# Performance work log

Measured on AMD Instinct MI355X. Metric: run time of the kernel, lower is better.

## Reference

```python
import jax, jax.numpy as jnp
import numpy as np

RC = 5.0          # radial cutoff
NB = 8            # number of Gaussian radial basis functions
NPATH = 11        # graph-conv tensor-product paths (in_way, r_way, n_contract)->out_way
NORM_FACTOR = 10.0


def setup_inputs() -> dict:
    key = jax.random.key(0)
    ks = jax.random.split(key, 24)
    N, E, C = 20000, 200000, 32
    s = 1.0 / np.sqrt(C)
    inp = {
        "rij": jax.random.normal(ks[0], (E, 3), jnp.float32) * 1.5,
        "node_x0": jax.random.normal(ks[1], (N, C), jnp.float32),
        "node_x1": jax.random.normal(ks[2], (N, C, 3), jnp.float32),
        "node_x2": jax.random.normal(ks[3], (N, C, 3, 3), jnp.float32),
        "idx_i": jax.random.randint(ks[4], (E,), 0, N, jnp.int32),
        "idx_j": jax.random.randint(ks[5], (E,), 0, N, jnp.int32),
        # radial filter MLP (rbf -> per-path per-channel filters)
        "W_rbf": jax.random.normal(ks[6], (NB, NPATH * C), jnp.float32) / np.sqrt(NB),
        "b_rbf": jax.random.normal(ks[7], (NPATH * C,), jnp.float32) * 0.1,
        # multi-body self-interaction: channel mixing per way + pair-path couplings
        "Wmix0": jax.random.normal(ks[8], (C, C), jnp.float32) * s,
        "Wmix1": jax.random.normal(ks[9], (C, C), jnp.float32) * s,
        "Wmix2": jax.random.normal(ks[10], (C, C), jnp.float32) * s,
        "coupling": jax.random.normal(ks[11], (8, C), jnp.float32) * 0.1,
        # gated nonlinearity params (gates computed from way-0 features)
        "Wg0": jax.random.normal(ks[12], (C, C), jnp.float32) * s,
        "Wg1": jax.random.normal(ks[13], (C, C), jnp.float32) * s,
        "Wg2": jax.random.normal(ks[14], (C, C), jnp.float32) * s,
        "bg0": jnp.zeros((C,), jnp.float32),
        "bg1": jnp.zeros((C,), jnp.float32),
        "bg2": jnp.zeros((C,), jnp.float32),
    }
    return inp


def _forward(rij, node_x0, node_x1, node_x2, idx_i, idx_j,
             W_rbf, b_rbf, Wmix0, Wmix1, Wmix2, coupling,
             Wg0, Wg1, Wg2, bg0, bg1, bg2):
    N, C = node_x0.shape
    # --- radial filters ---
    d = jnp.maximum(jnp.linalg.norm(rij, axis=-1), 1e-6)            # [E]
    rhat = rij / d[:, None]                                         # [E,3]
    centers = jnp.linspace(0.0, RC, NB)
    rbf = jnp.exp(-((d[:, None] - centers) ** 2) / 0.25)            # [E,NB]
    fc = 0.5 * (jnp.cos(jnp.pi * jnp.minimum(d, RC) / RC) + 1.0)    # cosine cutoff
    filt = ((rbf @ W_rbf + b_rbf) * fc[:, None]).reshape(-1, NPATH, C)  # [E,P,C]

    # --- graph conv (conv_mode='node_j'): gather neighbor tensors, tensor-product with rhat ---
    xj0 = node_x0[idx_j]                                            # [E,C]
    xj1 = node_x1[idx_j]                                            # [E,C,3]
    xj2 = node_x2[idx_j]                                            # [E,C,3,3]
    x1r = jnp.einsum('eca,ea->ec', xj1, rhat)                       # v.rhat

    m0 = filt[:, 0] * xj0
    m0 += filt[:, 5] * x1r
    m0 += filt[:, 10] * jnp.einsum('ecab,ea,eb->ec', xj2, rhat, rhat)

    m1 = jnp.einsum('ec,ea->eca', filt[:, 1] * xj0, rhat)
    m1 += filt[:, 3][:, :, None] * xj1
    m1 += jnp.einsum('ec,ea->eca', filt[:, 6] * x1r, rhat)
    m1 += filt[:, 8][:, :, None] * jnp.einsum('ecab,eb->eca', xj2, rhat)

    m2 = jnp.einsum('ec,ea,eb->ecab', filt[:, 2] * xj0, rhat, rhat)
    m2 += jnp.einsum('eca,eb->ecab', filt[:, 4][:, :, None] * xj1, rhat)
    m2 += filt[:, 7][:, :, None, None] * xj2
    m2 += filt[:, 9][:, :, None, None] * jnp.einsum('ecab,eb,ed->ecad', xj2, rhat, rhat)

    # --- scatter-add aggregation per way + normalization ---
    a0 = jax.ops.segment_sum(m0, idx_i, num_segments=N) / NORM_FACTOR
    a1 = jax.ops.segment_sum(m1, idx_i, num_segments=N) / NORM_FACTOR
    a2 = jax.ops.segment_sum(m2, idx_i, num_segments=N) / NORM_FACTOR

    # --- multi-body self-interaction (channel mix + pairwise tensor contractions) ---
    cp = coupling
    y0 = a0 @ Wmix0 \
        + cp[0] * (a0 * a0) \
        + cp[3] * jnp.einsum('nca,nca->nc', a1, a1) \
        + cp[6] * jnp.einsum('ncab,ncab->nc', a2, a2)
    y1 = jnp.einsum('nca,cd->nda', a1, Wmix1) \
        + cp[1][None, :, None] * a0[:, :, None] * a1 \
        + cp[5][None, :, None] * jnp.einsum('ncab,ncb->nca', a2, a1)
    y2 = jnp.einsum('ncab,cd->ndab', a2, Wmix2) \
        + cp[2][None, :, None, None] * a0[:, :, None, None] * a2 \
        + cp[4][None, :, None, None] * jnp.einsum('nca,ncb->ncab', a1, a1) \
        + cp[7][None, :, None, None] * jnp.einsum('ncab,ncbd->ncad', a2, a2)

    # --- gated nonlinearity (scalar channel drives gates for higher ways) ---
    z0 = jax.nn.silu(y0 @ Wg0 + bg0)
    z1 = y1 * jax.nn.silu(y0 @ Wg1 + bg1)[:, :, None]
    z2 = y2 * jax.nn.silu(y0 @ Wg2 + bg2)[:, :, None, None]

    # --- residual add (res_add) ---
    o0 = node_x0 + z0
    o1 = node_x1 + z1
    o2 = node_x2 + z2
    # pack dict {0,1,2} outputs into one array [N,C,1+3+9]
    return jnp.concatenate([o0[:, :, None], o1, o2.reshape(N, C, 9)], axis=-1)


def reference(rij, node_x0, node_x1, node_x2, idx_i, idx_j,
              W_rbf, b_rbf, Wmix0, Wmix1, Wmix2, coupling,
              Wg0, Wg1, Wg2, bg0, bg1, bg2):
    return _forward(rij, node_x0, node_x1, node_x2, idx_i, idx_j,
                    W_rbf, b_rbf, Wmix0, Wmix1, Wmix2, coupling,
                    Wg0, Wg1, Wg2, bg0, bg1, bg2)
```

## Files before the change

### kernel.cpp

```cpp
#include <hip/hip_runtime.h>
#include <cmath>

#define CH 32
#define NBASIS 8
#define NPATH 11
#define NF 13
#define NPF (NF * CH)
#define MAXDEG 40
#define NW 4

typedef unsigned int u32;
typedef __fp16 half2_t __attribute__((ext_vector_type(2)));

__device__ __forceinline__ float silu_f(float x) {
    return x / (1.0f + __expf(-x));
}

__device__ __forceinline__ u32 bf16r(float x) {
    return (__float_as_uint(x) + 0x8000u) >> 16;
}
__device__ __forceinline__ float bf16lo(u32 w) {
    return __uint_as_float(w << 16);
}
__device__ __forceinline__ float bf16hi(u32 w) {
    return __uint_as_float(w & 0xffff0000u);
}

__device__ __forceinline__ u32 f16pk(float a, float b) {
    union { half2_t h; u32 u; } cv;
    cv.h = __builtin_amdgcn_cvt_pkrtz(a, b);
    return cv.u;
}
__device__ __forceinline__ half2_t ash2(u32 w) {
    union { u32 u; half2_t h; } cv; cv.u = w; return cv.h;
}

#if __has_builtin(__builtin_amdgcn_fdot2)
__device__ __forceinline__ float dot2f(u32 a, u32 b, float c) {
    return __builtin_amdgcn_fdot2(ash2(a), ash2(b), c, false);
}
#else
__device__ __forceinline__ float dot2f(u32 a, u32 b, float c) {
    half2_t ha = ash2(a), hb = ash2(b);
    c = fmaf((float)ha.x, (float)hb.x, c);
    c = fmaf((float)ha.y, (float)hb.y, c);
    return c;
}
#endif

__device__ __forceinline__ void gload_lds16(const void* g, void* l) {
    __builtin_amdgcn_global_load_lds(
        (const __attribute__((address_space(1))) void*)g,
        (__attribute__((address_space(3))) void*)l, 16, 0, 0);
}

__global__ __launch_bounds__(256) void repack_kernel(
    const float* __restrict__ x0,
    const float* __restrict__ x1,
    const float* __restrict__ x2,
    uint4* __restrict__ xph4,
    int*   __restrict__ cnt,
    int N)
{
    int t = blockIdx.x * 256 + threadIdx.x;
    if (t < N) cnt[t] = 0;
    if (t >= N * CH) return;

    float f[13];
    f[0] = x0[t];
    const float* p1 = x1 + (size_t)t * 3;
#pragma unroll
    for (int a = 0; a < 3; a++) f[1 + a] = p1[a];
    const float* p2 = x2 + (size_t)t * 9;
#pragma unroll
    for (int q = 0; q < 9; q++) f[4 + q] = p2[q];

    u32 d[8];
#pragma unroll
    for (int qp = 0; qp < 6; qp++)
        d[qp] = bf16r(f[2 * qp]) | (bf16r(f[2 * qp + 1]) << 16);
    d[6] = bf16r(f[12]);
    d[7] = 0u;
    uint4* xo = xph4 + (size_t)t * 2;
    xo[0] = make_uint4(d[0], d[1], d[2], d[3]);
    xo[1] = make_uint4(d[4], d[5], d[6], d[7]);
}

__global__ __launch_bounds__(256) void fill_slots(
    const float* __restrict__ rij,
    const int*   __restrict__ idx_i,
    const int*   __restrict__ idx_j,
    int*    __restrict__ cnt,
    float4* __restrict__ recs,
    int E)
{
    int e = blockIdx.x * 256 + threadIdx.x;
    if (e >= E) return;

    float rx = rij[e * 3 + 0], ry = rij[e * 3 + 1], rz = rij[e * 3 + 2];
    float dn = sqrtf(rx * rx + ry * ry + rz * rz);
    float d = fmaxf(dn, 1e-6f);
    float inv = 1.0f / d;

    float rbf[NBASIS];
#pragma unroll
    for (int k = 0; k < NBASIS; k++) {
        float ck = 5.0f * (float)k / (float)(NBASIS - 1);
        float del = d - ck;
        rbf[k] = __expf(-4.0f * del * del);
    }
    float dc = fminf(d, 5.0f);
    float fc = 0.5f * (__cosf((float)M_PI * dc * 0.2f) + 1.0f);
    float scale = fc * 0.1f;

    int i = idx_i[e];
    int pos = atomicAdd(&cnt[i], 1);
    if (pos >= MAXDEG) return;

    u32 w3  = ((u32)idx_j[e] << 16) | bf16r(scale);
    u32 p01 = f16pk(rbf[0] * scale, rbf[1] * scale);
    u32 p23 = f16pk(rbf[2] * scale, rbf[3] * scale);
    u32 p45 = f16pk(rbf[4] * scale, rbf[5] * scale);
    u32 p67 = f16pk(rbf[6] * scale, rbf[7] * scale);

    float4* r = recs + 2 * (size_t)(i * MAXDEG + pos);
    r[0] = make_float4(rx * inv, ry * inv, rz * inv, __uint_as_float(w3));
    r[1] = make_float4(__uint_as_float(p01), __uint_as_float(p23),
                       __uint_as_float(p45), __uint_as_float(p67));
}

__global__ __launch_bounds__(256, 1) void edge_kernel(
    const float4*   __restrict__ recs,
    const uint4*    __restrict__ xph4,
    const int*      __restrict__ cnt,
    const float*    __restrict__ W_rbf,
    const float*    __restrict__ b_rbf,
    float* __restrict__ anode,
    int N)
{
    __shared__ uint4  sW4[NPATH * CH];
    __shared__ float4 srec[NW][MAXDEG * 2];

    int tid  = threadIdx.x;
    int wid  = tid >> 6;
    int lane = tid & 63;
    int half = lane >> 5;
    int c    = lane & 31;
    int n    = blockIdx.x * NW + wid;
    bool valid = (n < N);
    int nn = valid ? n : (N - 1);

    const char* gbase = (const char*)(recs + 2 * (size_t)nn * MAXDEG);
    {
        char* lbase = (char*)&srec[wid][0];
        gload_lds16(gbase + lane * 16, lbase);
        if (lane < 16)
            gload_lds16(gbase + 1024 + lane * 16, lbase + 1024);
    }

    const u32* recw = (const u32*)gbase;
    u32 w30 = recw[half * 8 + 3];
    u32 w31 = recw[(half + 2) * 8 + 3];
    u32 w32 = recw[(half + 4) * 8 + 3];
    int deg_g = cnt[nn];

#pragma unroll
    for (int i = 0; i < 2; i++) {
        int idx = tid + i * 256;
        if (idx < NPATH * CH) {
            int cc = idx & 31, p = idx >> 5;
            const float* w = W_rbf + p * CH + cc;
            uint4 v;
            v.x = f16pk(w[0 * NPATH * CH], w[1 * NPATH * CH]);
            v.y = f16pk(w[2 * NPATH * CH], w[3 * NPATH * CH]);
            v.z = f16pk(w[4 * NPATH * CH], w[5 * NPATH * CH]);
            v.w = f16pk(w[6 * NPATH * CH], w[7 * NPATH * CH]);
            sW4[idx] = v;
        }
    }

    float breg[NPATH];
#pragma unroll
    for (int p = 0; p < NPATH; p++) breg[p] = b_rbf[p * CH + c];

    auto gath = [&](uint4& ga, uint4& gb, u32 w3) {
        int j = (int)(w3 >> 16);
        j = j < N ? j : N - 1;
        const uint4* g = xph4 + (((size_t)j * CH + c) << 1);
        ga = g[0];
        gb = g[1];
    };

    uint4 G0a, G0b, G1a, G1b, G2a, G2b;
    gath(G0a, G0b, w30);
    gath(G1a, G1b, w31);
    gath(G2a, G2b, w32);

    __syncthreads();
    if (!valid) return;

    int deg = deg_g < MAXDEG ? deg_g : MAXDEG;

    int s0 = half, s1 = half + 2, s2 = half + 4;
    bool v0 = s0 < deg, v1 = s1 < deg, v2 = s2 < deg;

    float A0 = 0.0f, A1[3] = {0, 0, 0}, A2[9] = {0, 0, 0, 0, 0, 0, 0, 0, 0};

    const uint4* sW4c = sW4 + c;

    auto compute = [&](float4 ra, float4 rb4, uint4 ga, uint4 gb) {
        float G[13];
        G[0]  = bf16lo(ga.x); G[1]  = bf16hi(ga.x);
        G[2]  = bf16lo(ga.y); G[3]  = bf16hi(ga.y);
        G[4]  = bf16lo(ga.z); G[5]  = bf16hi(ga.z);
        G[6]  = bf16lo(ga.w); G[7]  = bf16hi(ga.w);
        G[8]  = bf16lo(gb.x); G[9]  = bf16hi(gb.x);
        G[10] = bf16lo(gb.y); G[11] = bf16hi(gb.y);
        G[12] = bf16lo(gb.z);

        float scale = bf16lo(__float_as_uint(ra.w));
        u32 pb0 = __float_as_uint(rb4.x), pb1 = __float_as_uint(rb4.y),
            pb2 = __float_as_uint(rb4.z), pb3 = __float_as_uint(rb4.w);

        float fv[NPATH];
#pragma unroll
        for (int p = 0; p < NPATH; p++) {
            uint4 wp = sW4c[p * CH];
            float acc = scale * breg[p];
            acc = dot2f(pb0, wp.x, acc);
            acc = dot2f(pb1, wp.y, acc);
            acc = dot2f(pb2, wp.z, acc);
            acc = dot2f(pb3, wp.w, acc);
            fv[p] = acc;
        }

        float hv[3] = {ra.x, ra.y, ra.z};
        float xj0 = G[0];
        float xv[3] = {G[1], G[2], G[3]};
        float x1r = xv[0] * hv[0] + xv[1] * hv[1] + xv[2] * hv[2];
        float x2r[3];
#pragma unroll
        for (int a = 0; a < 3; a++)
            x2r[a] = G[4 + a * 3 + 0] * hv[0] + G[4 + a * 3 + 1] * hv[1]
                   + G[4 + a * 3 + 2] * hv[2];
        float x2rr = x2r[0] * hv[0] + x2r[1] * hv[1] + x2r[2] * hv[2];

        A0 += fv[0] * xj0 + fv[5] * x1r + fv[10] * x2rr;

        float s01 = fv[1] * xj0 + fv[6] * x1r;
#pragma unroll
        for (int a = 0; a < 3; a++)
            A1[a] += s01 * hv[a] + fv[3] * xv[a] + fv[8] * x2r[a];

        float f2x = fv[2] * xj0;
#pragma unroll
        for (int a = 0; a < 3; a++) {
            float w = f2x * hv[a] + fv[4] * xv[a] + fv[9] * x2r[a];
#pragma unroll
            for (int b = 0; b < 3; b++)
                A2[a * 3 + b] += w * hv[b] + fv[7] * G[4 + a * 3 + b];
        }
    };

    const float4* sr = srec[wid];

    while (v0) {
        bool n0 = (s0 + 6 < deg);
        bool n1 = v1 && (s1 + 6 < deg);
        bool n2 = v2 && (s2 + 6 < deg);

        float4 ra0 = sr[2 * s0], rb0 = sr[2 * s0 + 1];
        int t0 = s0 + 6 < MAXDEG ? s0 + 6 : MAXDEG - 1;
        u32 w0n = __float_as_uint(sr[2 * t0].w);
        float4 ra1, rb1, ra2, rb2;
        u32 w1n = 0, w2n = 0;
        if (v1) {
            ra1 = sr[2 * s1]; rb1 = sr[2 * s1 + 1];
            int t1 = s1 + 6 < MAXDEG ? s1 + 6 : MAXDEG - 1;
            w1n = __float_as_uint(sr[2 * t1].w);
        }
        if (v2) {
            ra2 = sr[2 * s2]; rb2 = sr[2 * s2 + 1];
            int t2 = s2 + 6 < MAXDEG ? s2 + 6 : MAXDEG - 1;
            w2n = __float_as_uint(sr[2 * t2].w);
        }

        compute(ra0, rb0, G0a, G0b);
        if (n0) gath(G0a, G0b, w0n);
        s0 += 6; v0 = n0;

        if (v1) {
            compute(ra1, rb1, G1a, G1b);
            if (n1) gath(G1a, G1b, w1n);
            s1 += 6; v1 = n1;
        }
        if (v2) {
            compute(ra2, rb2, G2a, G2b);
            if (n2) gath(G2a, G2b, w2n);
            s2 += 6; v2 = n2;
        }
    }

    A0 += __shfl_xor(A0, 32);
#pragma unroll
    for (int a = 0; a < 3; a++) A1[a] += __shfl_xor(A1[a], 32);
#pragma unroll
    for (int q = 0; q < 9; q++) A2[q] += __shfl_xor(A2[q], 32);

    float* an = anode + (size_t)n * NPF;
    if (half == 0) {
        an[c] = A0;
#pragma unroll
        for (int a = 0; a < 3; a++) an[(1 + a) * CH + c] = A1[a];
    } else {
#pragma unroll
        for (int q = 0; q < 9; q++) an[(4 + q) * CH + c] = A2[q];
    }
}

__global__ __launch_bounds__(256) void node_update(
    const float* __restrict__ anode,
    const float* __restrict__ x0,
    const float* __restrict__ x1,
    const float* __restrict__ x2,
    const float* __restrict__ Wmix0, const float* __restrict__ Wmix1, const float* __restrict__ Wmix2,
    const float* __restrict__ coupling,
    const float* __restrict__ Wg0, const float* __restrict__ Wg1, const float* __restrict__ Wg2,
    const float* __restrict__ bg0, const float* __restrict__ bg1, const float* __restrict__ bg2,
    float* __restrict__ out, int N)
{
    __shared__ float sW[6][CH * CH];
    __shared__ float sA[8 * NPF];
    __shared__ float sy0[8][CH];
    __shared__ float ob[8 * NPF];

    int tid  = threadIdx.x;
    int nl   = tid >> 5;
    int d    = tid & 31;
    int nbase = blockIdx.x * 8;
    int n    = nbase + nl;
    int nsafe = n < N ? n : N - 1;

#pragma unroll
    for (int r = 0; r < 4; r++) {
        int idx = r * 256 + tid;
        sW[0][idx] = Wmix0[idx];
        sW[1][idx] = Wmix1[idx];
        sW[2][idx] = Wmix2[idx];
        sW[3][idx] = Wg0[idx];
        sW[4][idx] = Wg1[idx];
        sW[5][idx] = Wg2[idx];
    }
    int limit = (N - nbase) * NPF;
    if (limit > 8 * NPF) limit = 8 * NPF;
    {
        const float* ab = anode + (size_t)nbase * NPF;
#pragma unroll
        for (int r = 0; r < 13; r++) {
            int idx = r * 256 + tid;
            sA[idx] = (idx < limit) ? ab[idx] : 0.0f;
        }
    }
    __syncthreads();

    const float* An = sA + nl * NPF;

    float a0d = An[0 * CH + d];
    float a1d[3], a2d[9];
#pragma unroll
    for (int a = 0; a < 3; a++) a1d[a] = An[(1 + a) * CH + d];
#pragma unroll
    for (int q = 0; q < 9; q++) a2d[q] = An[(4 + q) * CH + d];

    float y0 = 0.0f;
#pragma unroll 8
    for (int cc = 0; cc < CH; cc++)
        y0 = fmaf(An[cc], sW[0][cc * CH + d], y0);
    {
        float cp0 = coupling[0 * CH + d], cp3 = coupling[3 * CH + d], cp6 = coupling[6 * CH + d];
        float n1v = a1d[0] * a1d[0] + a1d[1] * a1d[1] + a1d[2] * a1d[2];
        float n2v = 0.0f;
#pragma unroll
        for (int q = 0; q < 9; q++) n2v = fmaf(a2d[q], a2d[q], n2v);
        y0 += cp0 * a0d * a0d + cp3 * n1v + cp6 * n2v;
    }
    sy0[nl][d] = y0;
    __syncthreads();

    float y1[3] = {0, 0, 0};
    float y2[9] = {0, 0, 0, 0, 0, 0, 0, 0, 0};
    float g0 = bg0[d], g1 = bg1[d], g2 = bg2[d];
#pragma unroll 4
    for (int cc = 0; cc < CH; cc++) {
        float w1 = sW[1][cc * CH + d];
        float w2 = sW[2][cc * CH + d];
#pragma unroll
        for (int a = 0; a < 3; a++) y1[a] = fmaf(An[(1 + a) * CH + cc], w1, y1[a]);
#pragma unroll
        for (int q = 0; q < 9; q++) y2[q] = fmaf(An[(4 + q) * CH + cc], w2, y2[q]);
        float yv = sy0[nl][cc];
        g0 = fmaf(yv, sW[3][cc * CH + d], g0);
        g1 = fmaf(yv, sW[4][cc * CH + d], g1);
        g2 = fmaf(yv, sW[5][cc * CH + d], g2);
    }

    {
        float cp1 = coupling[1 * CH + d], cp5 = coupling[5 * CH + d];
#pragma unroll
        for (int a = 0; a < 3; a++) {
            float a2a1 = a2d[a * 3 + 0] * a1d[0] + a2d[a * 3 + 1] * a1d[1] + a2d[a * 3 + 2] * a1d[2];
            y1[a] += cp1 * a0d * a1d[a] + cp5 * a2a1;
        }
        float cp2 = coupling[2 * CH + d], cp4 = coupling[4 * CH + d], cp7 = coupling[7 * CH + d];
#pragma unroll
        for (int a = 0; a < 3; a++) {
#pragma unroll
            for (int b = 0; b < 3; b++) {
                float a2a2 = a2d[a * 3 + 0] * a2d[0 * 3 + b] + a2d[a * 3 + 1] * a2d[1 * 3 + b]
                           + a2d[a * 3 + 2] * a2d[2 * 3 + b];
                y2[a * 3 + b] += cp2 * a0d * a2d[a * 3 + b] + cp4 * a1d[a] * a1d[b] + cp7 * a2a2;
            }
        }
    }

    g0 = silu_f(g0);
    g1 = silu_f(g1);
    g2 = silu_f(g2);

    {
        const float* xs0 = x0 + (size_t)nsafe * CH;
        const float* xs1 = x1 + ((size_t)nsafe * CH + d) * 3;
        const float* xs2 = x2 + ((size_t)nsafe * CH + d) * 9;
        float* o = ob + nl * NPF + d * NF;
        o[0] = xs0[d] + g0;
#pragma unroll
        for (int a = 0; a < 3; a++)
            o[1 + a] = xs1[a] + y1[a] * g1;
#pragma unroll
        for (int q = 0; q < 9; q++)
            o[4 + q] = xs2[q] + y2[q] * g2;
    }
    __syncthreads();

    float* op = out + (size_t)nbase * NPF;
#pragma unroll
    for (int r = 0; r < 13; r++) {
        int idx = r * 256 + tid;
        if (idx < limit) op[idx] = ob[idx];
    }
}

extern "C" void kernel_launch(void* const* d_in, const int* in_sizes, int n_in,
                              void* d_out, int out_size, void* d_ws, size_t ws_size,
                              hipStream_t stream) {
    const float* rij      = (const float*)d_in[0];
    const float* x0       = (const float*)d_in[1];
    const float* x1       = (const float*)d_in[2];
    const float* x2       = (const float*)d_in[3];
    const int*   idx_i    = (const int*)d_in[4];
    const int*   idx_j    = (const int*)d_in[5];
    const float* W_rbf    = (const float*)d_in[6];
    const float* b_rbf    = (const float*)d_in[7];
    const float* Wmix0    = (const float*)d_in[8];
    const float* Wmix1    = (const float*)d_in[9];
    const float* Wmix2    = (const float*)d_in[10];
    const float* coupling = (const float*)d_in[11];
    const float* Wg0      = (const float*)d_in[12];
    const float* Wg1      = (const float*)d_in[13];
    const float* Wg2      = (const float*)d_in[14];
    const float* bg0      = (const float*)d_in[15];
    const float* bg1      = (const float*)d_in[16];
    const float* bg2      = (const float*)d_in[17];

    int E = in_sizes[4];
    int N = in_sizes[1] / CH;

    float4* recs  = (float4*)d_ws;
    uint4*  xph4  = (uint4*)(recs + 2 * (size_t)N * MAXDEG);
    int*    cnt   = (int*)(xph4 + (size_t)N * CH * 2);
    float*  anode = (float*)d_out;

    int ablocks = (N * CH + 255) / 256;
    repack_kernel<<<ablocks, 256, 0, stream>>>(x0, x1, x2, xph4, cnt, N);

    int eblocks = (E + 255) / 256;
    fill_slots<<<eblocks, 256, 0, stream>>>(rij, idx_i, idx_j, cnt, recs, E);

    edge_kernel<<<(N + NW - 1) / NW, 256, 0, stream>>>(recs, xph4, cnt,
                                                       W_rbf, b_rbf, anode, N);

    node_update<<<(N + 7) / 8, 256, 0, stream>>>(anode, x0, x1, x2,
                                                 Wmix0, Wmix1, Wmix2, coupling,
                                                 Wg0, Wg1, Wg2, bg0, bg1, bg2,
                                                 (float*)d_out, N);
}
```

Before: 223.7 us.

## Fuse all four stages into one persistent cooperative kernel with grid syncs

Replaces the repack, slot-fill, edge and node-update kernels with a single cooperative persistent kernel. Grid-wide syncs separate the phases, and a shared-memory buffer is reused across them. The aim is to remove launch overhead and inter-kernel gaps. In exchange it takes on grid-sync costs and limits occupancy to one block per CU, with launch_bounds(256,1) and large shared memory, for every phase. The node-update phase must now also run safely in place on the output buffer across persistent loops.

```diff
diff --git a/kernel.cpp b/kernel.cpp
--- a/kernel.cpp
+++ b/kernel.cpp
@@ -1,5 +1,8 @@
 #include <hip/hip_runtime.h>
+#include <hip/hip_cooperative_groups.h>
 #include <cmath>
+
+namespace cg = cooperative_groups;
 
 #define CH 32
 #define NBASIS 8
@@ -12,6 +15,16 @@
 typedef unsigned int u32;
 typedef __fp16 half2_t __attribute__((ext_vector_type(2)));
 
+#define SM_W4_BYTES   (NPATH * CH * 16)
+#define SM_SREC_OFF   SM_W4_BYTES
+#define SM_SREC_BYTES (NW * MAXDEG * 2 * 16)
+#define SM_W6_BYTES   (6 * CH * CH * 4)
+#define SM_SA_OFF     SM_W6_BYTES
+#define SM_SA_BYTES   (8 * NPF * 4)
+#define SM_SY0_OFF    (SM_SA_OFF + SM_SA_BYTES)
+#define SM_SY0_BYTES  (8 * CH * 4)
+#define SMEM_TOTAL    (SM_SY0_OFF + SM_SY0_BYTES)
+
 __device__ __forceinline__ float silu_f(float x) {
     return x / (1.0f + __expf(-x));
 }
@@ -54,399 +67,407 @@
         (__attribute__((address_space(3))) void*)l, 16, 0, 0);
 }
 
-__global__ __launch_bounds__(256) void repack_kernel(
+__global__ __launch_bounds__(256, 1) void mega_kernel(
+    const float* __restrict__ rij,
     const float* __restrict__ x0,
     const float* __restrict__ x1,
     const float* __restrict__ x2,
-    uint4* __restrict__ xph4,
-    int*   __restrict__ cnt,
-    int N)
-{
-    int t = blockIdx.x * 256 + threadIdx.x;
-    if (t < N) cnt[t] = 0;
-    if (t >= N * CH) return;
-
-    float f[13];
-    f[0] = x0[t];
-    const float* p1 = x1 + (size_t)t * 3;
-#pragma unroll
-    for (int a = 0; a < 3; a++) f[1 + a] = p1[a];
-    const float* p2 = x2 + (size_t)t * 9;
-#pragma unroll
-    for (int q = 0; q < 9; q++) f[4 + q] = p2[q];
-
-    u32 d[8];
-#pragma unroll
-    for (int qp = 0; qp < 6; qp++)
-        d[qp] = bf16r(f[2 * qp]) | (bf16r(f[2 * qp + 1]) << 16);
-    d[6] = bf16r(f[12]);
-    d[7] = 0u;
-    uint4* xo = xph4 + (size_t)t * 2;
-    xo[0] = make_uint4(d[0], d[1], d[2], d[3]);
-    xo[1] = make_uint4(d[4], d[5], d[6], d[7]);
-}
-
-__global__ __launch_bounds__(256) void fill_slots(
-    const float* __restrict__ rij,
     const int*   __restrict__ idx_i,
     const int*   __restrict__ idx_j,
+    const float* __restrict__ W_rbf,
+    const float* __restrict__ b_rbf,
+    const float* __restrict__ Wmix0, const float* __restrict__ Wmix1,
+    const float* __restrict__ Wmix2,
+    const float* __restrict__ coupling,
+    const float* __restrict__ Wg0, const float* __restrict__ Wg1,
+    const float* __restrict__ Wg2,
+    const float* __restrict__ bg0, const float* __restrict__ bg1,
+    const float* __restrict__ bg2,
+    float4* __restrict__ recs,
+    uint4*  __restrict__ xph4,
     int*    __restrict__ cnt,
-    float4* __restrict__ recs,
-    int E)
+    float*  __restrict__ out,
+    int N, int E)
 {
-    int e = blockIdx.x * 256 + threadIdx.x;
-    if (e >= E) return;
-
-    float rx = rij[e * 3 + 0], ry = rij[e * 3 + 1], rz = rij[e * 3 + 2];
-    float dn = sqrtf(rx * rx + ry * ry + rz * rz);
-    float d = fmaxf(dn, 1e-6f);
-    float inv = 1.0f / d;
-
-    float rbf[NBASIS];
-#pragma unroll
-    for (int k = 0; k < NBASIS; k++) {
-        float ck = 5.0f * (float)k / (float)(NBASIS - 1);
-        float del = d - ck;
-        rbf[k] = __expf(-4.0f * del * del);
+    cg::grid_group gg = cg::this_grid();
+    __shared__ __align__(16) char smem[SMEM_TOTAL];
+
+    int tid  = threadIdx.x;
+    int bid  = blockIdx.x;
+    int nblk = gridDim.x;
+    int gstride = nblk * 256;
+    int gt = bid * 256 + tid;
+
+    for (int i = gt; i < N; i += gstride) cnt[i] = 0;
+    gg.sync();
+
+    for (int t = gt; t < N * CH; t += gstride) {
+        float f[13];
+        f[0] = x0[t];
+        const float* p1 = x1 + (size_t)t * 3;
+#pragma unroll
+        for (int a = 0; a < 3; a++) f[1 + a] = p1[a];
+        const float* p2 = x2 + (size_t)t * 9;
+#pragma unroll
+        for (int q = 0; q < 9; q++) f[4 + q] = p2[q];
+
+        u32 d[8];
+#pragma unroll
+        for (int qp = 0; qp < 6; qp++)
+            d[qp] = bf16r(f[2 * qp]) | (bf16r(f[2 * qp + 1]) << 16);
+        d[6] = bf16r(f[12]);
+        d[7] = 0u;
+        uint4* xo = xph4 + (size_t)t * 2;
+        xo[0] = make_uint4(d[0], d[1], d[2], d[3]);
+        xo[1] = make_uint4(d[4], d[5], d[6], d[7]);
     }
-    float dc = fminf(d, 5.0f);
-    float fc = 0.5f * (__cosf((float)M_PI * dc * 0.2f) + 1.0f);
-    float scale = fc * 0.1f;
-
-    int i = idx_i[e];
-    int pos = atomicAdd(&cnt[i], 1);
-    if (pos >= MAXDEG) return;
-
-    u32 w3  = ((u32)idx_j[e] << 16) | bf16r(scale);
-    u32 p01 = f16pk(rbf[0] * scale, rbf[1] * scale);
-    u32 p23 = f16pk(rbf[2] * scale, rbf[3] * scale);
-    u32 p45 = f16pk(rbf[4] * scale, rbf[5] * scale);
-    u32 p67 = f16pk(rbf[6] * scale, rbf[7] * scale);
-
-    float4* r = recs + 2 * (size_t)(i * MAXDEG + pos);
-    r[0] = make_float4(rx * inv, ry * inv, rz * inv, __uint_as_float(w3));
-    r[1] = make_float4(__uint_as_float(p01), __uint_as_float(p23),
-                       __uint_as_float(p45), __uint_as_float(p67));
-}
-
-__global__ __launch_bounds__(256, 1) void edge_kernel(
-    const float4*   __restrict__ recs,
-    const uint4*    __restrict__ xph4,
-    const int*      __restrict__ cnt,
-    const float*    __restrict__ W_rbf,
-    const float*    __restrict__ b_rbf,
-    float* __restrict__ anode,
-    int N)
-{
-    __shared__ uint4  sW4[NPATH * CH];
-    __shared__ float4 srec[NW][MAXDEG * 2];
-
-    int tid  = threadIdx.x;
-    int wid  = tid >> 6;
-    int lane = tid & 63;
-    int half = lane >> 5;
-    int c    = lane & 31;
-    int n    = blockIdx.x * NW + wid;
-    bool valid = (n < N);
-    int nn = valid ? n : (N - 1);
-
-    const char* gbase = (const char*)(recs + 2 * (size_t)nn * MAXDEG);
+
+    for (int e = gt; e < E; e += gstride) {
+        float rx = rij[e * 3 + 0], ry = rij[e * 3 + 1], rz = rij[e * 3 + 2];
+        float dn = sqrtf(rx * rx + ry * ry + rz * rz);
+        float d = fmaxf(dn, 1e-6f);
+        float inv = 1.0f / d;
+
+        float rbf[NBASIS];
+#pragma unroll
+        for (int k = 0; k < NBASIS; k++) {
+            float ck = 5.0f * (float)k / (float)(NBASIS - 1);
+            float del = d - ck;
+            rbf[k] = __expf(-4.0f * del * del);
+        }
+        float dc = fminf(d, 5.0f);
+        float fc = 0.5f * (__cosf((float)M_PI * dc * 0.2f) + 1.0f);
+        float scale = fc * 0.1f;
+
+        int i = idx_i[e];
+        int pos = atomicAdd(&cnt[i], 1);
+        if (pos >= MAXDEG) continue;
+
+        u32 w3  = ((u32)idx_j[e] << 16) | bf16r(scale);
+        u32 p01 = f16pk(rbf[0] * scale, rbf[1] * scale);
+        u32 p23 = f16pk(rbf[2] * scale, rbf[3] * scale);
+        u32 p45 = f16pk(rbf[4] * scale, rbf[5] * scale);
+        u32 p67 = f16pk(rbf[6] * scale, rbf[7] * scale);
+
+        float4* r = recs + 2 * (size_t)(i * MAXDEG + pos);
+        r[0] = make_float4(rx * inv, ry * inv, rz * inv, __uint_as_float(w3));
+        r[1] = make_float4(__uint_as_float(p01), __uint_as_float(p23),
+                           __uint_as_float(p45), __uint_as_float(p67));
+    }
+    gg.sync();
+
     {
-        char* lbase = (char*)&srec[wid][0];
-        gload_lds16(gbase + lane * 16, lbase);
-        if (lane < 16)
-            gload_lds16(gbase + 1024 + lane * 16, lbase + 1024);
-    }
-
-    const u32* recw = (const u32*)gbase;
-    u32 w30 = recw[half * 8 + 3];
-    u32 w31 = recw[(half + 2) * 8 + 3];
-    u32 w32 = recw[(half + 4) * 8 + 3];
-    int deg_g = cnt[nn];
-
-#pragma unroll
-    for (int i = 0; i < 2; i++) {
-        int idx = tid + i * 256;
-        if (idx < NPATH * CH) {
-            int cc = idx & 31, p = idx >> 5;
+        uint4*  sW4  = (uint4*)smem;
+        float4* srec = (float4*)(smem + SM_SREC_OFF);
+
+        for (int i = tid; i < NPATH * CH; i += 256) {
+            int cc = i & 31, p = i >> 5;
             const float* w = W_rbf + p * CH + cc;
             uint4 v;
             v.x = f16pk(w[0 * NPATH * CH], w[1 * NPATH * CH]);
             v.y = f16pk(w[2 * NPATH * CH], w[3 * NPATH * CH]);
             v.z = f16pk(w[4 * NPATH * CH], w[5 * NPATH * CH]);
             v.w = f16pk(w[6 * NPATH * CH], w[7 * NPATH * CH]);
-            sW4[idx] = v;
+            sW4[i] = v;
+        }
+
+        int wid  = tid >> 6;
+        int lane = tid & 63;
+        int half = lane >> 5;
+        int c    = lane & 31;
+
+        float breg[NPATH];
+#pragma unroll
+        for (int p = 0; p < NPATH; p++) breg[p] = b_rbf[p * CH + c];
+
+        const uint4* sW4c = sW4 + c;
+        float4* srw = srec + (size_t)wid * (MAXDEG * 2);
+
+        auto gath = [&](uint4& ga, uint4& gb, u32 w3) {
+            int j = (int)(w3 >> 16);
+            j = j < N ? j : N - 1;
+            const uint4* g = xph4 + (((size_t)j * CH + c) << 1);
+            ga = g[0];
+            gb = g[1];
+        };
+
+        int ngroups = (N + NW - 1) / NW;
+        for (int g = bid; g < ngroups; g += nblk) {
+            __syncthreads();
+
+            int n = g * NW + wid;
+            bool valid = (n < N);
+            int nn = valid ? n : (N - 1);
+
+            const char* gbase = (const char*)(recs + 2 * (size_t)nn * MAXDEG);
+            {
+                char* lbase = (char*)srw;
+                gload_lds16(gbase + lane * 16, lbase);
+                if (lane < 16)
+                    gload_lds16(gbase + 1024 + lane * 16, lbase + 1024);
+            }
+
+            const u32* recw = (const u32*)gbase;
+            u32 w30 = recw[half * 8 + 3];
+            u32 w31 = recw[(half + 2) * 8 + 3];
+            u32 w32 = recw[(half + 4) * 8 + 3];
+            int deg_g = cnt[nn];
+
+            uint4 G0a, G0b, G1a, G1b, G2a, G2b;
+            gath(G0a, G0b, w30);
+            gath(G1a, G1b, w31);
+            gath(G2a, G2b, w32);
+
+            __syncthreads();
+
+            int deg = valid ? (deg_g < MAXDEG ? deg_g : MAXDEG) : 0;
+
+            int s0 = half, s1 = half + 2, s2 = half + 4;
+            bool v0 = s0 < deg, v1 = s1 < deg, v2 = s2 < deg;
+
+            float A0 = 0.0f, A1[3] = {0, 0, 0};
+            float A2[9] = {0, 0, 0, 0, 0, 0, 0, 0, 0};
+
+            auto compute = [&](float4 ra, float4 rb4, uint4 ga, uint4 gb) {
+                float G[13];
+                G[0]  = bf16lo(ga.x); G[1]  = bf16hi(ga.x);
+                G[2]  = bf16lo(ga.y); G[3]  = bf16hi(ga.y);
+                G[4]  = bf16lo(ga.z); G[5]  = bf16hi(ga.z);
+                G[6]  = bf16lo(ga.w); G[7]  = bf16hi(ga.w);
+                G[8]  = bf16lo(gb.x); G[9]  = bf16hi(gb.x);
+                G[10] = bf16lo(gb.y); G[11] = bf16hi(gb.y);
+                G[12] = bf16lo(gb.z);
+
+                float scale = bf16lo(__float_as_uint(ra.w));
+                u32 pb0 = __float_as_uint(rb4.x), pb1 = __float_as_uint(rb4.y),
+                    pb2 = __float_as_uint(rb4.z), pb3 = __float_as_uint(rb4.w);
+
+                float fv[NPATH];
+#pragma unroll
+                for (int p = 0; p < NPATH; p++) {
+                    uint4 wp = sW4c[p * CH];
+                    float acc = scale * breg[p];
+                    acc = dot2f(pb0, wp.x, acc);
+                    acc = dot2f(pb1, wp.y, acc);
+                    acc = dot2f(pb2, wp.z, acc);
+                    acc = dot2f(pb3, wp.w, acc);
+                    fv[p] = acc;
+                }
+
+                float hv[3] = {ra.x, ra.y, ra.z};
+                float xj0 = G[0];
+                float xv[3] = {G[1], G[2], G[3]};
+                float x1r = xv[0] * hv[0] + xv[1] * hv[1] + xv[2] * hv[2];
+                float x2r[3];
+#pragma unroll
+                for (int a = 0; a < 3; a++)
+                    x2r[a] = G[4 + a * 3 + 0] * hv[0] + G[4 + a * 3 + 1] * hv[1]
+                           + G[4 + a * 3 + 2] * hv[2];
+                float x2rr = x2r[0] * hv[0] + x2r[1] * hv[1] + x2r[2] * hv[2];
+
+                A0 += fv[0] * xj0 + fv[5] * x1r + fv[10] * x2rr;
+
+                float s01 = fv[1] * xj0 + fv[6] * x1r;
+#pragma unroll
+                for (int a = 0; a < 3; a++)
+                    A1[a] += s01 * hv[a] + fv[3] * xv[a] + fv[8] * x2r[a];
+
+                float f2x = fv[2] * xj0;
+#pragma unroll
+                for (int a = 0; a < 3; a++) {
+                    float w = f2x * hv[a] + fv[4] * xv[a] + fv[9] * x2r[a];
+#pragma unroll
+                    for (int b = 0; b < 3; b++)
+                        A2[a * 3 + b] += w * hv[b] + fv[7] * G[4 + a * 3 + b];
+                }
+            };
+
+            const float4* sr = srw;
+
+            while (v0) {
+                bool n0 = (s0 + 6 < deg);
+                bool n1 = v1 && (s1 + 6 < deg);
+                bool n2 = v2 && (s2 + 6 < deg);
+
+                float4 ra0 = sr[2 * s0], rb0 = sr[2 * s0 + 1];
+                int t0 = s0 + 6 < MAXDEG ? s0 + 6 : MAXDEG - 1;
+                u32 w0n = __float_as_uint(sr[2 * t0].w);
+                float4 ra1, rb1, ra2, rb2;
+                u32 w1n = 0, w2n = 0;
+                if (v1) {
+                    ra1 = sr[2 * s1]; rb1 = sr[2 * s1 + 1];
+                    int t1 = s1 + 6 < MAXDEG ? s1 + 6 : MAXDEG - 1;
+                    w1n = __float_as_uint(sr[2 * t1].w);
+                }
+                if (v2) {
+                    ra2 = sr[2 * s2]; rb2 = sr[2 * s2 + 1];
+                    int t2 = s2 + 6 < MAXDEG ? s2 + 6 : MAXDEG - 1;
+                    w2n = __float_as_uint(sr[2 * t2].w);
+                }
+
+                compute(ra0, rb0, G0a, G0b);
+                if (n0) gath(G0a, G0b, w0n);
+                s0 += 6; v0 = n0;
+
+                if (v1) {
+                    compute(ra1, rb1, G1a, G1b);
+                    if (n1) gath(G1a, G1b, w1n);
+                    s1 += 6; v1 = n1;
+                }
+                if (v2) {
+                    compute(ra2, rb2, G2a, G2b);
+                    if (n2) gath(G2a, G2b, w2n);
+                    s2 += 6; v2 = n2;
+                }
+            }
+
+            if (valid) {
+                A0 += __shfl_xor(A0, 32);
+#pragma unroll
+                for (int a = 0; a < 3; a++) A1[a] += __shfl_xor(A1[a], 32);
+#pragma unroll
+                for (int q = 0; q < 9; q++) A2[q] += __shfl_xor(A2[q], 32);
+
+                float* an = out + (size_t)n * NPF;
+                if (half == 0) {
+                    an[c] = A0;
+#pragma unroll
+                    for (int a = 0; a < 3; a++) an[(1 + a) * CH + c] = A1[a];
+                } else {
+#pragma unroll
+                    for (int q = 0; q < 9; q++) an[(4 + q) * CH + c] = A2[q];
+                }
+            }
         }
     }
-
-    float breg[NPATH];
-#pragma unroll
-    for (int p = 0; p < NPATH; p++) breg[p] = b_rbf[p * CH + c];
-
-    auto gath = [&](uint4& ga, uint4& gb, u32 w3) {
-        int j = (int)(w3 >> 16);
-        j = j < N ? j : N - 1;
-        const uint4* g = xph4 + (((size_t)j * CH + c) << 1);
-        ga = g[0];
-        gb = g[1];
-    };
-
-    uint4 G0a, G0b, G1a, G1b, G2a, G2b;
-    gath(G0a, G0b, w30);
-    gath(G1a, G1b, w31);
-    gath(G2a, G2b, w32);
-
-    __syncthreads();
-    if (!valid) return;
-
-    int deg = deg_g < MAXDEG ? deg_g : MAXDEG;
-
-    int s0 = half, s1 = half + 2, s2 = half + 4;
-    bool v0 = s0 < deg, v1 = s1 < deg, v2 = s2 < deg;
-
-    float A0 = 0.0f, A1[3] = {0, 0, 0}, A2[9] = {0, 0, 0, 0, 0, 0, 0, 0, 0};
-
-    const uint4* sW4c = sW4 + c;
-
-    auto compute = [&](float4 ra, float4 rb4, uint4 ga, uint4 gb) {
-        float G[13];
-        G[0]  = bf16lo(ga.x); G[1]  = bf16hi(ga.x);
-        G[2]  = bf16lo(ga.y); G[3]  = bf16hi(ga.y);
-        G[4]  = bf16lo(ga.z); G[5]  = bf16hi(ga.z);
-        G[6]  = bf16lo(ga.w); G[7]  = bf16hi(ga.w);
-        G[8]  = bf16lo(gb.x); G[9]  = bf16hi(gb.x);
-        G[10] = bf16lo(gb.y); G[11] = bf16hi(gb.y);
-        G[12] = bf16lo(gb.z);
-
-        float scale = bf16lo(__float_as_uint(ra.w));
-        u32 pb0 = __float_as_uint(rb4.x), pb1 = __float_as_uint(rb4.y),
-            pb2 = __float_as_uint(rb4.z), pb3 = __float_as_uint(rb4.w);
-
-        float fv[NPATH];
-#pragma unroll
-        for (int p = 0; p < NPATH; p++) {
-            uint4 wp = sW4c[p * CH];
-            float acc = scale * breg[p];
-            acc = dot2f(pb0, wp.x, acc);
-            acc = dot2f(pb1, wp.y, acc);
-            acc = dot2f(pb2, wp.z, acc);
-            acc = dot2f(pb3, wp.w, acc);
-            fv[p] = acc;
+    gg.sync();
+
+    {
+        float* sW6  = (float*)smem;
+        float* sA   = (float*)(smem + SM_SA_OFF);
+        float* sy0v = (float*)(smem + SM_SY0_OFF);
+
+#pragma unroll
+        for (int r = 0; r < 4; r++) {
+            int idx = r * 256 + tid;
+            sW6[0 * 1024 + idx] = Wmix0[idx];
+            sW6[1 * 1024 + idx] = Wmix1[idx];
+            sW6[2 * 1024 + idx] = Wmix2[idx];
+            sW6[3 * 1024 + idx] = Wg0[idx];
+            sW6[4 * 1024 + idx] = Wg1[idx];
+            sW6[5 * 1024 + idx] = Wg2[idx];
         }
 
-        float hv[3] = {ra.x, ra.y, ra.z};
-        float xj0 = G[0];
-        float xv[3] = {G[1], G[2], G[3]};
-        float x1r = xv[0] * hv[0] + xv[1] * hv[1] + xv[2] * hv[2];
-        float x2r[3];
-#pragma unroll
-        for (int a = 0; a < 3; a++)
-            x2r[a] = G[4 + a * 3 + 0] * hv[0] + G[4 + a * 3 + 1] * hv[1]
-                   + G[4 + a * 3 + 2] * hv[2];
-        float x2rr = x2r[0] * hv[0] + x2r[1] * hv[1] + x2r[2] * hv[2];
-
-        A0 += fv[0] * xj0 + fv[5] * x1r + fv[10] * x2rr;
-
-        float s01 = fv[1] * xj0 + fv[6] * x1r;
-#pragma unroll
-        for (int a = 0; a < 3; a++)
-            A1[a] += s01 * hv[a] + fv[3] * xv[a] + fv[8] * x2r[a];
-
-        float f2x = fv[2] * xj0;
-#pragma unroll
-        for (int a = 0; a < 3; a++) {
-            float w = f2x * hv[a] + fv[4] * xv[a] + fv[9] * x2r[a];
-#pragma unroll
-            for (int b = 0; b < 3; b++)
-                A2[a * 3 + b] += w * hv[b] + fv[7] * G[4 + a * 3 + b];
+        int nl = tid >> 5;
+        int d  = tid & 31;
+
+        int noct = (N + 7) / 8;
+        for (int g = bid; g < noct; g += nblk) {
+            __syncthreads();
+
+            int nbase = g * 8;
+            int n     = nbase + nl;
+            int nsafe = n < N ? n : N - 1;
+            int limit = (N - nbase) * NPF;
+            if (limit > 8 * NPF) limit = 8 * NPF;
+
+            const float* ab = out + (size_t)nbase * NPF;
+#pragma unroll
+            for (int r = 0; r < 13; r++) {
+                int idx = r * 256 + tid;
+                sA[idx] = (idx < limit) ? ab[idx] : 0.0f;
+            }
+            __syncthreads();
+
+            const float* An = sA + nl * NPF;
+
+            float a0d = An[0 * CH + d];
+            float a1d[3], a2d[9];
+#pragma unroll
+            for (int a = 0; a < 3; a++) a1d[a] = An[(1 + a) * CH + d];
+#pragma unroll
+            for (int q = 0; q < 9; q++) a2d[q] = An[(4 + q) * CH + d];
+
+            float y0 = 0.0f;
+#pragma unroll 8
+            for (int cc = 0; cc < CH; cc++)
+                y0 = fmaf(An[cc], sW6[0 * 1024 + cc * CH + d], y0);
+            {
+                float cp0 = coupling[0 * CH + d], cp3 = coupling[3 * CH + d],
+                      cp6 = coupling[6 * CH + d];
+                float n1v = a1d[0] * a1d[0] + a1d[1] * a1d[1] + a1d[2] * a1d[2];
+                float n2v = 0.0f;
+#pragma unroll
+                for (int q = 0; q < 9; q++) n2v = fmaf(a2d[q], a2d[q], n2v);
+                y0 += cp0 * a0d * a0d + cp3 * n1v + cp6 * n2v;
+            }
+            sy0v[nl * CH + d] = y0;
+            __syncthreads();
+
+            float y1[3] = {0, 0, 0};
+            float y2[9] = {0, 0, 0, 0, 0, 0, 0, 0, 0};
+            float g0 = bg0[d], g1 = bg1[d], g2 = bg2[d];
+#pragma unroll 4
+            for (int cc = 0; cc < CH; cc++) {
+                float w1 = sW6[1 * 1024 + cc * CH + d];
+                float w2 = sW6[2 * 1024 + cc * CH + d];
+#pragma unroll
+                for (int a = 0; a < 3; a++)
+                    y1[a] = fmaf(An[(1 + a) * CH + cc], w1, y1[a]);
+#pragma unroll
+                for (int q = 0; q < 9; q++)
+                    y2[q] = fmaf(An[(4 + q) * CH + cc], w2, y2[q]);
+                float yv = sy0v[nl * CH + cc];
+                g0 = fmaf(yv, sW6[3 * 1024 + cc * CH + d], g0);
+                g1 = fmaf(yv, sW6[4 * 1024 + cc * CH + d], g1);
+                g2 = fmaf(yv, sW6[5 * 1024 + cc * CH + d], g2);
+            }
+
+            {
+                float cp1 = coupling[1 * CH + d], cp5 = coupling[5 * CH + d];
+#pragma unroll
+                for (int a = 0; a < 3; a++) {
+                    float a2a1 = a2d[a * 3 + 0] * a1d[0] + a2d[a * 3 + 1] * a1d[1]
+                               + a2d[a * 3 + 2] * a1d[2];
+                    y1[a] += cp1 * a0d * a1d[a] + cp5 * a2a1;
+                }
+                float cp2 = coupling[2 * CH + d], cp4 = coupling[4 * CH + d],
+                      cp7 = coupling[7 * CH + d];
+#pragma unroll
+                for (int a = 0; a < 3; a++) {
+#pragma unroll
+                    for (int b = 0; b < 3; b++) {
+                        float a2a2 = a2d[a * 3 + 0] * a2d[0 * 3 + b]
+                                   + a2d[a * 3 + 1] * a2d[1 * 3 + b]
+                                   + a2d[a * 3 + 2] * a2d[2 * 3 + b];
+                        y2[a * 3 + b] += cp2 * a0d * a2d[a * 3 + b]
+                                       + cp4 * a1d[a] * a1d[b] + cp7 * a2a2;
+                    }
+                }
+            }
+
+            g0 = silu_f(g0);
+            g1 = silu_f(g1);
+            g2 = silu_f(g2);
+
+            if (n < N) {
+                const float* xs0 = x0 + (size_t)nsafe * CH;
+                const float* xs1 = x1 + ((size_t)nsafe * CH + d) * 3;
+                const float* xs2 = x2 + ((size_t)nsafe * CH + d) * 9;
+                float* o = out + (size_t)n * NPF + d * NF;
+                float r0 = xs0[d] + g0;
+                float r1[3], r2[9];
+#pragma unroll
+                for (int a = 0; a < 3; a++) r1[a] = xs1[a] + y1[a] * g1;
+#pragma unroll
+                for (int q = 0; q < 9; q++) r2[q] = xs2[q] + y2[q] * g2;
+                o[0] = r0;
+#pragma unroll
+                for (int a = 0; a < 3; a++) o[1 + a] = r1[a];
+#pragma unroll
+                for (int q = 0; q < 9; q++) o[4 + q] = r2[q];
+            }
         }
-    };
-
-    const float4* sr = srec[wid];
-
-    while (v0) {
-        bool n0 = (s0 + 6 < deg);
-        bool n1 = v1 && (s1 + 6 < deg);
-        bool n2 = v2 && (s2 + 6 < deg);
-
-        float4 ra0 = sr[2 * s0], rb0 = sr[2 * s0 + 1];
-        int t0 = s0 + 6 < MAXDEG ? s0 + 6 : MAXDEG - 1;
-        u32 w0n = __float_as_uint(sr[2 * t0].w);
-        float4 ra1, rb1, ra2, rb2;
-        u32 w1n = 0, w2n = 0;
-        if (v1) {
-            ra1 = sr[2 * s1]; rb1 = sr[2 * s1 + 1];
-            int t1 = s1 + 6 < MAXDEG ? s1 + 6 : MAXDEG - 1;
-            w1n = __float_as_uint(sr[2 * t1].w);
-        }
-        if (v2) {
-            ra2 = sr[2 * s2]; rb2 = sr[2 * s2 + 1];
-            int t2 = s2 + 6 < MAXDEG ? s2 + 6 : MAXDEG - 1;
-            w2n = __float_as_uint(sr[2 * t2].w);
-        }
-
-        compute(ra0, rb0, G0a, G0b);
-        if (n0) gath(G0a, G0b, w0n);
-        s0 += 6; v0 = n0;
-
-        if (v1) {
-            compute(ra1, rb1, G1a, G1b);
-            if (n1) gath(G1a, G1b, w1n);
-            s1 += 6; v1 = n1;
-        }
-        if (v2) {
-            compute(ra2, rb2, G2a, G2b);
-            if (n2) gath(G2a, G2b, w2n);
-            s2 += 6; v2 = n2;
-        }
-    }
-
-    A0 += __shfl_xor(A0, 32);
-#pragma unroll
-    for (int a = 0; a < 3; a++) A1[a] += __shfl_xor(A1[a], 32);
-#pragma unroll
-    for (int q = 0; q < 9; q++) A2[q] += __shfl_xor(A2[q], 32);
-
-    float* an = anode + (size_t)n * NPF;
-    if (half == 0) {
-        an[c] = A0;
-#pragma unroll
-        for (int a = 0; a < 3; a++) an[(1 + a) * CH + c] = A1[a];
-    } else {
-#pragma unroll
-        for (int q = 0; q < 9; q++) an[(4 + q) * CH + c] = A2[q];
-    }
-}
-
-__global__ __launch_bounds__(256) void node_update(
-    const float* __restrict__ anode,
-    const float* __restrict__ x0,
-    const float* __restrict__ x1,
-    const float* __restrict__ x2,
-    const float* __restrict__ Wmix0, const float* __restrict__ Wmix1, const float* __restrict__ Wmix2,
-    const float* __restrict__ coupling,
-    const float* __restrict__ Wg0, const float* __restrict__ Wg1, const float* __restrict__ Wg2,
-    const float* __restrict__ bg0, const float* __restrict__ bg1, const float* __restrict__ bg2,
-    float* __restrict__ out, int N)
-{
-    __shared__ float sW[6][CH * CH];
-    __shared__ float sA[8 * NPF];
-    __shared__ float sy0[8][CH];
-    __shared__ float ob[8 * NPF];
-
-    int tid  = threadIdx.x;
-    int nl   = tid >> 5;
-    int d    = tid & 31;
-    int nbase = blockIdx.x * 8;
-    int n    = nbase + nl;
-    int nsafe = n < N ? n : N - 1;
-
-#pragma unroll
-    for (int r = 0; r < 4; r++) {
-        int idx = r * 256 + tid;
-        sW[0][idx] = Wmix0[idx];
-        sW[1][idx] = Wmix1[idx];
-        sW[2][idx] = Wmix2[idx];
-        sW[3][idx] = Wg0[idx];
-        sW[4][idx] = Wg1[idx];
-        sW[5][idx] = Wg2[idx];
-    }
-    int limit = (N - nbase) * NPF;
-    if (limit > 8 * NPF) limit = 8 * NPF;
-    {
-        const float* ab = anode + (size_t)nbase * NPF;
-#pragma unroll
-        for (int r = 0; r < 13; r++) {
-            int idx = r * 256 + tid;
-            sA[idx] = (idx < limit) ? ab[idx] : 0.0f;
-        }
-    }
-    __syncthreads();
-
-    const float* An = sA + nl * NPF;
-
-    float a0d = An[0 * CH + d];
-    float a1d[3], a2d[9];
-#pragma unroll
-    for (int a = 0; a < 3; a++) a1d[a] = An[(1 + a) * CH + d];
-#pragma unroll
-    for (int q = 0; q < 9; q++) a2d[q] = An[(4 + q) * CH + d];
-
-    float y0 = 0.0f;
-#pragma unroll 8
-    for (int cc = 0; cc < CH; cc++)
-        y0 = fmaf(An[cc], sW[0][cc * CH + d], y0);
-    {
-        float cp0 = coupling[0 * CH + d], cp3 = coupling[3 * CH + d], cp6 = coupling[6 * CH + d];
-        float n1v = a1d[0] * a1d[0] + a1d[1] * a1d[1] + a1d[2] * a1d[2];
-        float n2v = 0.0f;
-#pragma unroll
-        for (int q = 0; q < 9; q++) n2v = fmaf(a2d[q], a2d[q], n2v);
-        y0 += cp0 * a0d * a0d + cp3 * n1v + cp6 * n2v;
-    }
-    sy0[nl][d] = y0;
-    __syncthreads();
-
-    float y1[3] = {0, 0, 0};
-    float y2[9] = {0, 0, 0, 0, 0, 0, 0, 0, 0};
-    float g0 = bg0[d], g1 = bg1[d], g2 = bg2[d];
-#pragma unroll 4
-    for (int cc = 0; cc < CH; cc++) {
-        float w1 = sW[1][cc * CH + d];
-        float w2 = sW[2][cc * CH + d];
-#pragma unroll
-        for (int a = 0; a < 3; a++) y1[a] = fmaf(An[(1 + a) * CH + cc], w1, y1[a]);
-#pragma unroll
-        for (int q = 0; q < 9; q++) y2[q] = fmaf(An[(4 + q) * CH + cc], w2, y2[q]);
-        float yv = sy0[nl][cc];
-        g0 = fmaf(yv, sW[3][cc * CH + d], g0);
-        g1 = fmaf(yv, sW[4][cc * CH + d], g1);
-        g2 = fmaf(yv, sW[5][cc * CH + d], g2);
-    }
-
-    {
-        float cp1 = coupling[1 * CH + d], cp5 = coupling[5 * CH + d];
-#pragma unroll
-        for (int a = 0; a < 3; a++) {
-            float a2a1 = a2d[a * 3 + 0] * a1d[0] + a2d[a * 3 + 1] * a1d[1] + a2d[a * 3 + 2] * a1d[2];
-            y1[a] += cp1 * a0d * a1d[a] + cp5 * a2a1;
-        }
-        float cp2 = coupling[2 * CH + d], cp4 = coupling[4 * CH + d], cp7 = coupling[7 * CH + d];
-#pragma unroll
-        for (int a = 0; a < 3; a++) {
-#pragma unroll
-            for (int b = 0; b < 3; b++) {
-                float a2a2 = a2d[a * 3 + 0] * a2d[0 * 3 + b] + a2d[a * 3 + 1] * a2d[1 * 3 + b]
-                           + a2d[a * 3 + 2] * a2d[2 * 3 + b];
-                y2[a * 3 + b] += cp2 * a0d * a2d[a * 3 + b] + cp4 * a1d[a] * a1d[b] + cp7 * a2a2;
-            }
-        }
-    }
-
-    g0 = silu_f(g0);
-    g1 = silu_f(g1);
-    g2 = silu_f(g2);
-
-    {
-        const float* xs0 = x0 + (size_t)nsafe * CH;
-        const float* xs1 = x1 + ((size_t)nsafe * CH + d) * 3;
-        const float* xs2 = x2 + ((size_t)nsafe * CH + d) * 9;
-        float* o = ob + nl * NPF + d * NF;
-        o[0] = xs0[d] + g0;
-#pragma unroll
-        for (int a = 0; a < 3; a++)
-            o[1 + a] = xs1[a] + y1[a] * g1;
-#pragma unroll
-        for (int q = 0; q < 9; q++)
-            o[4 + q] = xs2[q] + y2[q] * g2;
-    }
-    __syncthreads();
-
-    float* op = out + (size_t)nbase * NPF;
-#pragma unroll
-    for (int r = 0; r < 13; r++) {
-        int idx = r * 256 + tid;
-        if (idx < limit) op[idx] = ob[idx];
     }
 }
 
@@ -475,22 +496,38 @@
     int E = in_sizes[4];
     int N = in_sizes[1] / CH;
 
-    float4* recs  = (float4*)d_ws;
-    uint4*  xph4  = (uint4*)(recs + 2 * (size_t)N * MAXDEG);
-    int*    cnt   = (int*)(xph4 + (size_t)N * CH * 2);
-    float*  anode = (float*)d_out;
-
-    int ablocks = (N * CH + 255) / 256;
-    repack_kernel<<<ablocks, 256, 0, stream>>>(x0, x1, x2, xph4, cnt, N);
-
-    int eblocks = (E + 255) / 256;
-    fill_slots<<<eblocks, 256, 0, stream>>>(rij, idx_i, idx_j, cnt, recs, E);
-
-    edge_kernel<<<(N + NW - 1) / NW, 256, 0, stream>>>(recs, xph4, cnt,
-                                                       W_rbf, b_rbf, anode, N);
-
-    node_update<<<(N + 7) / 8, 256, 0, stream>>>(anode, x0, x1, x2,
-                                                 Wmix0, Wmix1, Wmix2, coupling,
-                                                 Wg0, Wg1, Wg2, bg0, bg1, bg2,
-                                                 (float*)d_out, N);
-}
+    float4* recs = (float4*)d_ws;
+    uint4*  xph4 = (uint4*)(recs + 2 * (size_t)N * MAXDEG);
+    int*    cnt  = (int*)(xph4 + (size_t)N * CH * 2);
+    float*  outp = (float*)d_out;
+
+    static int gridBlocks = 0;
+    if (gridBlocks == 0) {
+        int maxB = 0;
+        hipOccupancyMaxActiveBlocksPerMultiprocessor(&maxB, mega_kernel, 256, 0);
+        if (maxB < 1) maxB = 1;
+        int ncu = 256;
+        hipDeviceProp_t prop;
+        int dev = 0;
+        if (hipGetDevice(&dev) == hipSuccess &&
+            hipGetDeviceProperties(&prop, dev) == hipSuccess &&
+            prop.multiProcessorCount > 0)
+            ncu = prop.multiProcessorCount;
+        gridBlocks = maxB * ncu;
+    }
+
+    void* args[] = {
+        (void*)&rij, (void*)&x0, (void*)&x1, (void*)&x2,
+        (void*)&idx_i, (void*)&idx_j,
+        (void*)&W_rbf, (void*)&b_rbf,
+        (void*)&Wmix0, (void*)&Wmix1, (void*)&Wmix2,
+        (void*)&coupling,
+        (void*)&Wg0, (void*)&Wg1, (void*)&Wg2,
+        (void*)&bg0, (void*)&bg1, (void*)&bg2,
+        (void*)&recs, (void*)&xph4, (void*)&cnt,
+        (void*)&outp, (void*)&N, (void*)&E
+    };
+
+    hipLaunchCooperativeKernel(mega_kernel, dim3(gridBlocks), dim3(256),
+                               args, 0, stream);
+}
```

Result: slower. 405.5 us (+81.2%).
